# Optimization experiments

Hardware: AMD Instinct MI355X
Metric: run time of the kernel (lower is better)

The kernel has to match this reference:

```python
import jax, jax.numpy as jnp
import numpy as np

EPS = 1e-6

def masked_softmax(x, m, axis):
    # Faithful to KrantikariQA tensor_utils.masked_softmax:
    #   x = x*m; e = exp(x - max(x)) * m; e / (sum(e) + 1e-6)
    x = x * m
    ex = jnp.exp(x - jnp.max(x, axis=axis, keepdims=True)) * m
    return ex / (jnp.sum(ex, axis=axis, keepdims=True) + EPS)

def setup_inputs() -> dict:
    key = jax.random.key(0)
    k = jax.random.split(key, 7)
    Lq, Lp, B, D = 256, 256, 64, 1024
    q = jax.random.normal(k[0], (Lq, B, D), jnp.float32)
    p = jax.random.normal(k[1], (Lp, B, D), jnp.float32)
    qm = jax.random.randint(k[2], (B, Lq), 0, 2).astype(jnp.int32)
    pm = jax.random.randint(k[3], (B, Lp), 0, 2).astype(jnp.int32)
    # nn.Linear weights (out, in), no bias
    WF = jax.random.normal(k[4], (D, D), jnp.float32) * 0.02
    WG = jax.random.normal(k[5], (D, 2 * D), jnp.float32) * 0.02
    WH = jax.random.normal(k[6], (1, 2 * D), jnp.float32) * 0.02
    return {"q": q, "p": p, "qm": qm, "pm": pm, "WF": WF, "WG": WG, "WH": WH}

def reference(q, p, qm, pm, WF, WG, WH):
    # Attend: att = F(x), batch-first [B, L, D]
    att_q = jnp.einsum('lbd,ed->ble', q, WF)          # [B,Lq,D]
    att_p = jnp.einsum('lbd,ed->ble', p, WF)          # [B,Lp,D]
    e = jnp.einsum('bqe,bpe->bqp', att_q, att_p)      # [B,Lq,Lp]
    m = qm.astype(q.dtype)[:, :, None] * pm.astype(q.dtype)[:, None, :]  # [B,Lq,Lp]
    softmax_j = masked_softmax(e, m, axis=2)                              # over Lp
    softmax_i = masked_softmax(e.transpose(0, 2, 1), m.transpose(0, 2, 1), axis=2)  # [B,Lp,Lq]
    beta = jnp.einsum('bqp,pbd->bqd', softmax_j, p)   # [B,Lq,D]
    alpha = jnp.einsum('bpq,qbd->bpd', softmax_i, q)  # [B,Lp,D]
    # Compare
    v1 = jnp.concatenate([q.transpose(1, 0, 2), beta], axis=-1) @ WG.T   # [B,Lq,D]
    v2 = jnp.concatenate([p.transpose(1, 0, 2), alpha], axis=-1) @ WG.T  # [B,Lp,D]
    # Aggregate
    sum_v1 = jnp.sum(v1, axis=1)  # [B,D]
    sum_v2 = jnp.sum(v2, axis=1)  # [B,D]
    return jnp.concatenate([sum_v1, sum_v2], axis=-1) @ WH.T  # [B,1]
```

## Files before the change

kernel.cpp:

```cpp
#include <hip/hip_runtime.h>

typedef _Float16 f16x8 __attribute__((ext_vector_type(8)));
using f32x4 = __attribute__((ext_vector_type(4))) float;

constexpr int B = 64, L = 256, D = 1024;
constexpr int BD = B * D;
constexpr float EPS = 1e-6f;

__device__ __forceinline__ void gload_lds16(const void* g, void* l) {
    __builtin_amdgcn_global_load_lds((const __attribute__((address_space(1))) void*)g,
                                     (__attribute__((address_space(3))) void*)l,
                                     16, 0, 0);
}

__global__ __launch_bounds__(256) void k_wfgp(const float* __restrict__ WF,
                                              const float* __restrict__ WG,
                                              const float* __restrict__ WH,
                                              short* __restrict__ WFt16,
                                              float* __restrict__ gp1,
                                              float* __restrict__ gp2) {
    __shared__ float tile[32][33];
    const int bid = blockIdx.x;
    if (bid < 1024) {
        const int rt = bid >> 5, ct = bid & 31;
        const int t = threadIdx.x;
        const int r = t >> 3, c4 = (t & 7) * 4;
        float4 v = *(const float4*)(WF + (long)(rt * 32 + r) * D + ct * 32 + c4);
        tile[r][c4] = v.x; tile[r][c4 + 1] = v.y; tile[r][c4 + 2] = v.z; tile[r][c4 + 3] = v.w;
        __syncthreads();
        union { _Float16 h[4]; short4 s; } u;
        u.h[0] = (_Float16)tile[c4 + 0][r];
        u.h[1] = (_Float16)tile[c4 + 1][r];
        u.h[2] = (_Float16)tile[c4 + 2][r];
        u.h[3] = (_Float16)tile[c4 + 3][r];
        *(short4*)(WFt16 + (long)(ct * 32 + r) * D + rt * 32 + c4) = u.s;
    } else {
        const int lb = bid - 1024;
        const int kx = lb & 7, ec = lb >> 3;
        const int k = kx * 256 + threadIdx.x;
        const int e0 = ec * 128;
        float a = 0.f, c = 0.f;
        for (int e = 0; e < 128; ++e) {
            float w = WG[(long)(e0 + e) * (2 * D) + k];
            a += w * WH[e0 + e];
            c += w * WH[D + e0 + e];
        }
        gp1[ec * 2048 + k] = a; gp2[ec * 2048 + k] = c;
    }
}

template <int WM, int WN, int MR, int A32, int B32>
__global__ __launch_bounds__(WM * WN * 64) void k_gemm(
    const char* __restrict__ A, long sA, long bA,
    const char* __restrict__ Bm, long sB, long bB,
    int K, int bx, int per_batch, int f16_out,
    short* __restrict__ Ch, float* __restrict__ Cf, int ldC, long batchC)
{
    constexpr int BM = WM * MR * 16, BN = WN * 64;
    constexpr int T = WM * WN * 64;
    constexpr int TILEB = (BM + BN) * 64;
    constexpr int ROUNDS = TILEB / (T * 16);
    constexpr int ROUNDS_A = (BM * 4) / T;
    constexpr int R0 = A32 ? 0 : ROUNDS_A;
    constexpr int R1 = A32 ? ROUNDS_A : (B32 ? ROUNDS : ROUNDS_A);
    constexpr int NR = (R1 > R0) ? (R1 - R0) : 1;
    __shared__ __align__(16) char lds[2 * TILEB];

    const int t = threadIdx.x, lane = t & 63, w = t >> 6;
    const int wm = w / WN, wn = w % WN;

    const int lin = blockIdx.x;
    const int chunk = gridDim.x >> 3;
    const int swz = (lin & 7) * chunk + (lin >> 3);
    const int z = swz / per_batch;
    const int r0_ = swz % per_batch;
    const int mb = (r0_ / bx) * BM, nb = (r0_ % bx) * BN;

    const char* Ab = A + bA * z;
    const char* Bb = Bm + bB * z;

    const char* sp[ROUNDS];
    #pragma unroll
    for (int r = 0; r < ROUNDS; ++r) {
        int g = r * T + t;
        int row = g >> 2, sg = g & 3;
        int lg = sg ^ ((row >> 1) & 3);
        if (r < ROUNDS_A) sp[r] = Ab + (long)(mb + row) * sA + lg * (A32 ? 32 : 16);
        else              sp[r] = Bb + (long)(nb + row - BM) * sB + lg * (B32 ? 32 : 16);
    }

    int aoff[MR], boff[4];
    #pragma unroll
    for (int i = 0; i < MR; ++i) {
        int ra = wm * (MR * 16) + i * 16 + (lane & 15);
        aoff[i] = ra * 64 + (((lane >> 4) ^ ((ra >> 1) & 3))) * 16;
    }
    #pragma unroll
    for (int j = 0; j < 4; ++j) {
        int rb = wn * 64 + j * 16 + (lane & 15);
        boff[j] = BM * 64 + rb * 64 + (((lane >> 4) ^ ((rb >> 1) & 3))) * 16;
    }

    f32x4 acc[MR][4] = {};
    const int NT = K >> 5;
    int cur = 0;

#define CVT8(U, S0, S1)                                                     \
    U.h[0]=(_Float16)S0.x; U.h[1]=(_Float16)S0.y;                           \
    U.h[2]=(_Float16)S0.z; U.h[3]=(_Float16)S0.w;                           \
    U.h[4]=(_Float16)S1.x; U.h[5]=(_Float16)S1.y;                           \
    U.h[6]=(_Float16)S1.z; U.h[7]=(_Float16)S1.w;

#define GSTEP(WSRC, LDST, KT)                                               \
    {                                                                       \
        asm volatile("s_waitcnt vmcnt(0)" ::: "memory");                    \
        __builtin_amdgcn_sched_barrier(0);                                  \
        __builtin_amdgcn_s_barrier();                                       \
        __builtin_amdgcn_sched_barrier(0);                                  \
        char* dstb = lds + (cur ^ 1) * TILEB;                               \
        if ((KT) + 2 < NT) {                                                \
            long kb = (long)((KT) + 2) * 128;                               \
            _Pragma("unroll")                                               \
            for (int r = R0; r < R1; ++r) {                                 \
                LDST[r - R0][0] = *(const float4*)(sp[r] + kb);             \
                LDST[r - R0][1] = *(const float4*)(sp[r] + kb + 16);        \
            }                                                               \
        }                                                                   \
        if ((KT) + 1 < NT) {                                                \
            long kb16 = (long)((KT) + 1) * 64;                              \
            _Pragma("unroll")                                               \
            for (int r = 0; r < ROUNDS; ++r)                                \
                if (r < R0 || r >= R1)                                      \
                    gload_lds16(sp[r] + kb16, dstb + (r * T + t) * 16);     \
            _Pragma("unroll")                                               \
            for (int r = R0; r < R1; ++r) {                                 \
                union { _Float16 h[8]; int4 v; } u;                         \
                float4 s0 = WSRC[r - R0][0], s1 = WSRC[r - R0][1];          \
                CVT8(u, s0, s1)                                             \
                *((int4*)(dstb + (r * T + t) * 16)) = u.v;                  \
            }                                                               \
        }                                                                   \
        __builtin_amdgcn_sched_barrier(0);                                  \
        const char* lb = lds + cur * TILEB;                                 \
        f16x8 fb[4], fa[MR];                                                \
        _Pragma("unroll")                                                   \
        for (int j = 0; j < 4; ++j) fb[j] = *(const f16x8*)(lb + boff[j]);  \
        _Pragma("unroll")                                                   \
        for (int i = 0; i < MR; ++i) fa[i] = *(const f16x8*)(lb + aoff[i]); \
        _Pragma("unroll")                                                   \
        for (int i = 0; i < MR; ++i)                                        \
            _Pragma("unroll")                                               \
            for (int j = 0; j < 4; ++j)                                     \
                acc[i][j] = __builtin_amdgcn_mfma_f32_16x16x32_f16(         \
                    fb[j], fa[i], acc[i][j], 0, 0, 0);                      \
        asm volatile("s_waitcnt lgkmcnt(0)" ::: "memory");                  \
        __builtin_amdgcn_sched_barrier(0);                                  \
        cur ^= 1;                                                           \
    }

    if constexpr (A32 || B32) {
        float4 rsA[NR][2], rsB[NR][2];
        #pragma unroll
        for (int r = 0; r < ROUNDS; ++r) {
            if (r >= R0 && r < R1) {
                float4 s0 = *(const float4*)(sp[r]);
                float4 s1 = *(const float4*)(sp[r] + 16);
                union { _Float16 h[8]; int4 v; } u;
                CVT8(u, s0, s1)
                *((int4*)(lds + (r * T + t) * 16)) = u.v;
            } else {
                gload_lds16(sp[r], lds + (r * T + t) * 16);
            }
        }
        if (NT > 1) {
            #pragma unroll
            for (int r = R0; r < R1; ++r) {
                rsB[r - R0][0] = *(const float4*)(sp[r] + 128);
                rsB[r - R0][1] = *(const float4*)(sp[r] + 128 + 16);
            }
        }
        asm volatile("s_waitcnt lgkmcnt(0)" ::: "memory");
        for (int kt = 0; kt < NT; kt += 2) {
            GSTEP(rsB, rsA, kt)
            GSTEP(rsA, rsB, kt + 1)
        }
    } else {
        #pragma unroll
        for (int r = 0; r < ROUNDS; ++r)
            gload_lds16(sp[r], lds + (r * T + t) * 16);
        for (int kt = 0; kt < NT; ++kt) {
            asm volatile("s_waitcnt vmcnt(0)" ::: "memory");
            __builtin_amdgcn_sched_barrier(0);
            __builtin_amdgcn_s_barrier();
            __builtin_amdgcn_sched_barrier(0);
            if (kt + 1 < NT) {
                long kb = (long)(kt + 1) * 64;
                char* dstb = lds + (cur ^ 1) * TILEB;
                #pragma unroll
                for (int r = 0; r < ROUNDS; ++r)
                    gload_lds16(sp[r] + kb, dstb + (r * T + t) * 16);
            }
            __builtin_amdgcn_sched_barrier(0);
            const char* lb = lds + cur * TILEB;
            f16x8 fb[4], fa[MR];
            #pragma unroll
            for (int j = 0; j < 4; ++j) fb[j] = *(const f16x8*)(lb + boff[j]);
            #pragma unroll
            for (int i = 0; i < MR; ++i) fa[i] = *(const f16x8*)(lb + aoff[i]);
            #pragma unroll
            for (int i = 0; i < MR; ++i)
                #pragma unroll
                for (int j = 0; j < 4; ++j)
                    acc[i][j] = __builtin_amdgcn_mfma_f32_16x16x32_f16(fb[j], fa[i], acc[i][j], 0, 0, 0);
            cur ^= 1;
        }
    }
#undef GSTEP
#undef CVT8

    const long zC = batchC * z;
    #pragma unroll
    for (int i = 0; i < MR; ++i)
        #pragma unroll
        for (int j = 0; j < 4; ++j) {
            int row = mb + wm * (MR * 16) + i * 16 + (lane & 15);
            int col = nb + wn * 64 + j * 16 + (lane >> 4) * 4;
            long idx = zC + (long)row * ldC + col;
            if (f16_out) {
                union { _Float16 h[4]; short4 s; } u;
                #pragma unroll
                for (int rr = 0; rr < 4; ++rr) u.h[rr] = (_Float16)acc[i][j][rr];
                *(short4*)(Ch + idx) = u.s;
            } else {
                float4 v = make_float4(acc[i][j][0], acc[i][j][1], acc[i][j][2], acc[i][j][3]);
                *(float4*)(Cf + idx) = v;
            }
        }
}

__global__ __launch_bounds__(256) void k_fold_g(const float* __restrict__ Gp,
                                                short* __restrict__ G16) {
    const int i = blockIdx.x * 256 + threadIdx.x;
    constexpr int N4 = (1 << 20) / 4;
    const float4* g = (const float4*)Gp;
    float4 v0 = g[i], v1 = g[N4 + i], v2 = g[2 * N4 + i], v3 = g[3 * N4 + i];
    union { _Float16 h[4]; short4 s; } u;
    u.h[0] = (_Float16)(v0.x + v1.x + v2.x + v3.x);
    u.h[1] = (_Float16)(v0.y + v1.y + v2.y + v3.y);
    u.h[2] = (_Float16)(v0.z + v1.z + v2.z + v3.z);
    u.h[3] = (_Float16)(v0.w + v1.w + v2.w + v3.w);
    ((short4*)G16)[i] = u.s;
}

__global__ __launch_bounds__(256) void k_pass1(const float* __restrict__ E,
                                               const int* __restrict__ qm,
                                               const int* __restrict__ pm,
                                               float* __restrict__ impart,
                                               float* __restrict__ ispart,
                                               float* __restrict__ cjpart) {
    const int qc = blockIdx.x, b = blockIdx.y;
    const int p = threadIdx.x, lane = p & 63, w = p >> 6;
    const int q0 = qc * 32;
    __shared__ float wred[32][4];
    __shared__ float rowmx[32], rowsm[32], qmv_s[32];
    if (p < 32) qmv_s[p] = (float)qm[b * L + q0 + p];
    __syncthreads();
    const float pmv = (float)pm[b * L + p];
    const float* eb = E + b * (L * L) + q0 * L + p;

    float xv[32];
    float im = -1e30f;
    #pragma unroll
    for (int r = 0; r < 32; ++r) {
        float mm = pmv * qmv_s[r];
        float x = eb[r * L] * mm;
        xv[r] = x;
        im = fmaxf(im, x);
        float v = x;
        #pragma unroll
        for (int o = 32; o; o >>= 1) v = fmaxf(v, __shfl_xor(v, o));
        if (lane == 0) wred[r][w] = v;
    }
    __syncthreads();
    if (p < 32) rowmx[p] = fmaxf(fmaxf(wred[p][0], wred[p][1]), fmaxf(wred[p][2], wred[p][3]));
    __syncthreads();
    float is = 0.f;
    #pragma unroll
    for (int r = 0; r < 32; ++r) {
        float mm = pmv * qmv_s[r];
        is += mm * __expf(xv[r] - im);
        float v = mm * __expf(xv[r] - rowmx[r]);
        #pragma unroll
        for (int o = 32; o; o >>= 1) v += __shfl_xor(v, o);
        if (lane == 0) wred[r][w] = v;
    }
    __syncthreads();
    if (p < 32) rowsm[p] = wred[p][0] + wred[p][1] + wred[p][2] + wred[p][3];
    __syncthreads();
    float cj = 0.f;
    #pragma unroll
    for (int r = 0; r < 32; ++r) {
        float mm = pmv * qmv_s[r];
        cj += mm * __expf(xv[r] - rowmx[r]) / (rowsm[r] + EPS);
    }
    const int o = (b * 8 + qc) * 256 + p;
    impart[o] = im; ispart[o] = is; cjpart[o] = cj;
}

__global__ __launch_bounds__(256) void k_combine(const float* __restrict__ impart,
                                                 const float* __restrict__ ispart,
                                                 const float* __restrict__ cjpart,
                                                 float* __restrict__ rmi,
                                                 float* __restrict__ rsi,
                                                 float* __restrict__ colj) {
    const int b = blockIdx.x, p = threadIdx.x;
    const int base = b * 8 * 256 + p;
    float m = -1e30f, s = 0.f, c = 0.f;
    #pragma unroll
    for (int k = 0; k < 8; ++k) m = fmaxf(m, impart[base + k * 256]);
    #pragma unroll
    for (int k = 0; k < 8; ++k) {
        s += ispart[base + k * 256] * __expf(impart[base + k * 256] - m);
        c += cjpart[base + k * 256];
    }
    rmi[b * L + p] = m; rsi[b * L + p] = s; colj[b * L + p] = c;
}

__global__ __launch_bounds__(256) void k_colsum_i(const float* __restrict__ E,
                                                  const int* __restrict__ qm,
                                                  const int* __restrict__ pm,
                                                  const float* __restrict__ rmaxi,
                                                  const float* __restrict__ rsumi,
                                                  float* __restrict__ coli) {
    const int wid = threadIdx.x >> 6, lane = threadIdx.x & 63;
    const int row = blockIdx.x * 4 + wid;
    const int b = row >> 8;
    const float qmv = (float)qm[row];
    const float* er = E + row * L;
    float acc = 0.f;
    #pragma unroll
    for (int i = 0; i < 4; ++i) {
        int pp = lane + 64 * i;
        float mm = qmv * (float)pm[b * L + pp];
        float x = er[pp] * mm;
        acc += mm * __expf(x - rmaxi[b * L + pp]) / (rsumi[b * L + pp] + EPS);
    }
    #pragma unroll
    for (int o = 32; o; o >>= 1) acc += __shfl_xor(acc, o);
    if (lane == 0) coli[row] = acc;
}

__global__ __launch_bounds__(128) void k_sums2(const float* __restrict__ Q,
                                               const float* __restrict__ P,
                                               const float* __restrict__ colj,
                                               const float* __restrict__ coli,
                                               float* __restrict__ pq,
                                               float* __restrict__ pp,
                                               float* __restrict__ pb,
                                               float* __restrict__ pa) {
    const int c = blockIdx.x, b = blockIdx.y, t = threadIdx.x;
    const int d0 = t * 8;
    float aq[8] = {}, ap[8] = {}, ab[8] = {}, aa[8] = {};
    for (int l = c * 16; l < c * 16 + 16; ++l) {
        const float* qp = Q + (long)l * BD + b * D + d0;
        const float* pp_ = P + (long)l * BD + b * D + d0;
        float4 q0 = *(const float4*)qp, q1 = *(const float4*)(qp + 4);
        float4 p0 = *(const float4*)pp_, p1 = *(const float4*)(pp_ + 4);
        float cj = colj[b * L + l], ci = coli[b * L + l];
        float qv[8] = {q0.x, q0.y, q0.z, q0.w, q1.x, q1.y, q1.z, q1.w};
        float pv[8] = {p0.x, p0.y, p0.z, p0.w, p1.x, p1.y, p1.z, p1.w};
        #pragma unroll
        for (int k = 0; k < 8; ++k) {
            aq[k] += qv[k]; ap[k] += pv[k]; ab[k] += cj * pv[k]; aa[k] += ci * qv[k];
        }
    }
    const long o = ((long)c * B + b) * D + d0;
    *(float4*)(pq + o) = make_float4(aq[0], aq[1], aq[2], aq[3]);
    *(float4*)(pq + o + 4) = make_float4(aq[4], aq[5], aq[6], aq[7]);
    *(float4*)(pp + o) = make_float4(ap[0], ap[1], ap[2], ap[3]);
    *(float4*)(pp + o + 4) = make_float4(ap[4], ap[5], ap[6], ap[7]);
    *(float4*)(pb + o) = make_float4(ab[0], ab[1], ab[2], ab[3]);
    *(float4*)(pb + o + 4) = make_float4(ab[4], ab[5], ab[6], ab[7]);
    *(float4*)(pa + o) = make_float4(aa[0], aa[1], aa[2], aa[3]);
    *(float4*)(pa + o + 4) = make_float4(aa[4], aa[5], aa[6], aa[7]);
}

__global__ __launch_bounds__(256) void k_final2(const float* __restrict__ pq,
                                                const float* __restrict__ pp,
                                                const float* __restrict__ pb,
                                                const float* __restrict__ pa,
                                                const float* __restrict__ gp1,
                                                const float* __restrict__ gp2,
                                                float* __restrict__ out) {
    const int b = blockIdx.x, t = threadIdx.x;
    float acc = 0.f;
    for (int d = t; d < D; d += 256) {
        float sq = 0.f, sp_ = 0.f, sb = 0.f, sa = 0.f;
        #pragma unroll
        for (int c2 = 0; c2 < 16; ++c2) {
            long o = ((long)c2 * B + b) * D + d;
            sq += pq[o]; sp_ += pp[o]; sb += pb[o]; sa += pa[o];
        }
        float g1d = 0.f, g1D = 0.f, g2d = 0.f, g2D = 0.f;
        #pragma unroll
        for (int ec = 0; ec < 8; ++ec) {
            g1d += gp1[ec * 2048 + d];     g1D += gp1[ec * 2048 + D + d];
            g2d += gp2[ec * 2048 + d];     g2D += gp2[ec * 2048 + D + d];
        }
        acc += sq * g1d + sb * g1D + sp_ * g2d + sa * g2D;
    }
    #pragma unroll
    for (int o = 32; o; o >>= 1) acc += __shfl_xor(acc, o);
    __shared__ float red[4];
    const int wid = t >> 6, lane = t & 63;
    if (lane == 0) red[wid] = acc;
    __syncthreads();
    if (t == 0) out[b] = red[0] + red[1] + red[2] + red[3];
}

extern "C" void kernel_launch(void* const* d_in, const int* in_sizes, int n_in,
                              void* d_out, int out_size, void* d_ws, size_t ws_size,
                              hipStream_t stream) {
    const float* q  = (const float*)d_in[0];
    const float* p  = (const float*)d_in[1];
    const int*   qm = (const int*)d_in[2];
    const int*   pm = (const int*)d_in[3];
    const float* WF = (const float*)d_in[4];
    const float* WG = (const float*)d_in[5];
    const float* WH = (const float*)d_in[6];
    float* out = (float*)d_out;

    char* wsb = (char*)d_ws;
    short* T16   = (short*)(wsb);
    short* WFt16 = (short*)(wsb + (32l << 20));
    short* G16   = (short*)(wsb + (34l << 20));
    float* Gp    = (float*)(wsb + (36l << 20));
    float* E     = (float*)(wsb + (36l << 20));
    float* st    = (float*)(wsb + (52l << 20));
    const int BL = B * L;
    float* impart = st;                  float* ispart = impart + B * 8 * 256;
    float* cjpart = ispart + B * 8 * 256;
    float* rmi  = cjpart + B * 8 * 256;  float* rsi  = rmi + BL;
    float* colj = rsi + BL;              float* coli = colj + BL;
    float* pq   = coli + BL;             float* pp   = pq + 16 * BD;
    float* pb   = pp + 16 * BD;          float* pa   = pb + 16 * BD;
    float* gp1  = pa + 16 * BD;          float* gp2  = gp1 + 8 * 2048;

    k_wfgp<<<1088, 256, 0, stream>>>(WF, WG, WH, WFt16, gp1, gp2);
    k_gemm<2, 2, 4, 0, 0><<<256, 256, 0, stream>>>(
        (const char*)WFt16, 2048, 512, (const char*)WFt16, 2048, 512,
        256, 8, 64, 0, nullptr, Gp, 1024, 1l << 20);
    k_fold_g<<<1024, 256, 0, stream>>>(Gp, G16);
    k_gemm<2, 4, 8, 1, 0><<<256, 512, 0, stream>>>(
        (const char*)q, 4096, 0, (const char*)G16, 2048, 0,
        1024, 4, 256, 1, T16, nullptr, 1024, 0);
    k_gemm<2, 2, 4, 0, 1><<<256, 256, 0, stream>>>(
        (const char*)T16, 64l * 2048, 2048, (const char*)p, 64l * 4096, 4096,
        1024, 2, 4, 0, nullptr, E, 256, 65536);
    k_pass1<<<dim3(8, B), 256, 0, stream>>>(E, qm, pm, impart, ispart, cjpart);
    k_combine<<<B, 256, 0, stream>>>(impart, ispart, cjpart, rmi, rsi, colj);
    k_colsum_i<<<BL / 4, 256, 0, stream>>>(E, qm, pm, rmi, rsi, coli);
    k_sums2<<<dim3(16, B), 128, 0, stream>>>(q, p, colj, coli, pq, pp, pb, pa);
    k_final2<<<B, 256, 0, stream>>>(pq, pp, pb, pa, gp1, gp2, out);
}
```

Baseline: 190.2 us.

## Triple-buffer GEMM LDS pipeline with two-tile lookahead and partial vmcnt waits

Replaces the double-buffered GEMM main loop with a three-stage LDS ring. Loads are issued two k-tiles ahead, and the loop waits with a partial vmcnt so the next tile's loads stay in flight during compute. The fp32 register-staged convert path and the direct global-to-LDS path now share one loop. In exchange it uses 50% more LDS per block, which may reduce occupancy, and it relies on hard-coded vmcnt counts matching the number of issued loads.

```diff
diff --git a/kernel.cpp b/kernel.cpp
--- a/kernel.cpp
+++ b/kernel.cpp
@@ -63,8 +63,11 @@
     constexpr int ROUNDS_A = (BM * 4) / T;
     constexpr int R0 = A32 ? 0 : ROUNDS_A;
     constexpr int R1 = A32 ? ROUNDS_A : (B32 ? ROUNDS : ROUNDS_A);
-    constexpr int NR = (R1 > R0) ? (R1 - R0) : 1;
-    __shared__ __align__(16) char lds[2 * TILEB];
+    constexpr int NF32 = (R1 > R0) ? (R1 - R0) : 0;
+    constexpr int NRS = NF32 ? NF32 : 1;
+    constexpr int VSET = (ROUNDS - NF32) + 2 * NF32;
+    static_assert(VSET == 4 || VSET == 6, "vmcnt literal dispatch");
+    __shared__ __align__(16) char lds[3 * TILEB];
 
     const int t = threadIdx.x, lane = t & 63, w = t >> 6;
     const int wm = w / WN, wn = w % WN;
@@ -103,45 +106,43 @@
 
     f32x4 acc[MR][4] = {};
     const int NT = K >> 5;
-    int cur = 0;
-
-#define CVT8(U, S0, S1)                                                     \
-    U.h[0]=(_Float16)S0.x; U.h[1]=(_Float16)S0.y;                           \
-    U.h[2]=(_Float16)S0.z; U.h[3]=(_Float16)S0.w;                           \
-    U.h[4]=(_Float16)S1.x; U.h[5]=(_Float16)S1.y;                           \
-    U.h[6]=(_Float16)S1.z; U.h[7]=(_Float16)S1.w;
-
-#define GSTEP(WSRC, LDST, KT)                                               \
+    float4 rsE[NRS][2], rsO[NRS][2];
+
+#define ISSUE(KT, RS)                                                       \
     {                                                                       \
-        asm volatile("s_waitcnt vmcnt(0)" ::: "memory");                    \
+        char* dstb = lds + ((KT) % 3) * TILEB;                              \
+        long kb16 = (long)(KT) * 64, kb32 = (long)(KT) * 128;               \
+        _Pragma("unroll")                                                   \
+        for (int r = 0; r < ROUNDS; ++r)                                    \
+            if (r < R0 || r >= R1)                                          \
+                gload_lds16(sp[r] + kb16, dstb + (r * T + t) * 16);         \
+        _Pragma("unroll")                                                   \
+        for (int r = R0; r < R1; ++r) {                                     \
+            RS[r - R0][0] = *(const float4*)(sp[r] + kb32);                 \
+            RS[r - R0][1] = *(const float4*)(sp[r] + kb32 + 16);            \
+        }                                                                   \
+    }
+
+#define CVTW(KT, RS)                                                        \
+    if (NF32) {                                                             \
+        char* dstb = lds + ((KT) % 3) * TILEB;                              \
+        _Pragma("unroll")                                                   \
+        for (int r = R0; r < R1; ++r) {                                     \
+            union { _Float16 h[8]; int4 v; } u;                             \
+            float4 s0 = RS[r - R0][0], s1 = RS[r - R0][1];                  \
+            u.h[0]=(_Float16)s0.x; u.h[1]=(_Float16)s0.y;                   \
+            u.h[2]=(_Float16)s0.z; u.h[3]=(_Float16)s0.w;                   \
+            u.h[4]=(_Float16)s1.x; u.h[5]=(_Float16)s1.y;                   \
+            u.h[6]=(_Float16)s1.z; u.h[7]=(_Float16)s1.w;                   \
+            *((int4*)(dstb + (r * T + t) * 16)) = u.v;                      \
+        }                                                                   \
+        asm volatile("s_waitcnt lgkmcnt(0)" ::: "memory");                  \
         __builtin_amdgcn_sched_barrier(0);                                  \
-        __builtin_amdgcn_s_barrier();                                       \
-        __builtin_amdgcn_sched_barrier(0);                                  \
-        char* dstb = lds + (cur ^ 1) * TILEB;                               \
-        if ((KT) + 2 < NT) {                                                \
-            long kb = (long)((KT) + 2) * 128;                               \
-            _Pragma("unroll")                                               \
-            for (int r = R0; r < R1; ++r) {                                 \
-                LDST[r - R0][0] = *(const float4*)(sp[r] + kb);             \
-                LDST[r - R0][1] = *(const float4*)(sp[r] + kb + 16);        \
-            }                                                               \
-        }                                                                   \
-        if ((KT) + 1 < NT) {                                                \
-            long kb16 = (long)((KT) + 1) * 64;                              \
-            _Pragma("unroll")                                               \
-            for (int r = 0; r < ROUNDS; ++r)                                \
-                if (r < R0 || r >= R1)                                      \
-                    gload_lds16(sp[r] + kb16, dstb + (r * T + t) * 16);     \
-            _Pragma("unroll")                                               \
-            for (int r = R0; r < R1; ++r) {                                 \
-                union { _Float16 h[8]; int4 v; } u;                         \
-                float4 s0 = WSRC[r - R0][0], s1 = WSRC[r - R0][1];          \
-                CVT8(u, s0, s1)                                             \
-                *((int4*)(dstb + (r * T + t) * 16)) = u.v;                  \
-            }                                                               \
-        }                                                                   \
-        __builtin_amdgcn_sched_barrier(0);                                  \
-        const char* lb = lds + cur * TILEB;                                 \
+    }
+
+#define COMPUTE(KT)                                                         \
+    {                                                                       \
+        const char* lb = lds + ((KT) % 3) * TILEB;                          \
         f16x8 fb[4], fa[MR];                                                \
         _Pragma("unroll")                                                   \
         for (int j = 0; j < 4; ++j) fb[j] = *(const f16x8*)(lb + boff[j]);  \
@@ -153,70 +154,37 @@
             for (int j = 0; j < 4; ++j)                                     \
                 acc[i][j] = __builtin_amdgcn_mfma_f32_16x16x32_f16(         \
                     fb[j], fa[i], acc[i][j], 0, 0, 0);                      \
-        asm volatile("s_waitcnt lgkmcnt(0)" ::: "memory");                  \
+    }
+
+#define STEP(KT, RS)                                                        \
+    {                                                                       \
+        if ((KT) + 1 < NT) {                                                \
+            if constexpr (VSET == 4)                                        \
+                asm volatile("s_waitcnt vmcnt(4)" ::: "memory");            \
+            else                                                            \
+                asm volatile("s_waitcnt vmcnt(6)" ::: "memory");            \
+        } else {                                                            \
+            asm volatile("s_waitcnt vmcnt(0)" ::: "memory");                \
+        }                                                                   \
         __builtin_amdgcn_sched_barrier(0);                                  \
-        cur ^= 1;                                                           \
-    }
-
-    if constexpr (A32 || B32) {
-        float4 rsA[NR][2], rsB[NR][2];
-        #pragma unroll
-        for (int r = 0; r < ROUNDS; ++r) {
-            if (r >= R0 && r < R1) {
-                float4 s0 = *(const float4*)(sp[r]);
-                float4 s1 = *(const float4*)(sp[r] + 16);
-                union { _Float16 h[8]; int4 v; } u;
-                CVT8(u, s0, s1)
-                *((int4*)(lds + (r * T + t) * 16)) = u.v;
-            } else {
-                gload_lds16(sp[r], lds + (r * T + t) * 16);
-            }
-        }
-        if (NT > 1) {
-            #pragma unroll
-            for (int r = R0; r < R1; ++r) {
-                rsB[r - R0][0] = *(const float4*)(sp[r] + 128);
-                rsB[r - R0][1] = *(const float4*)(sp[r] + 128 + 16);
-            }
-        }
-        asm volatile("s_waitcnt lgkmcnt(0)" ::: "memory");
-        for (int kt = 0; kt < NT; kt += 2) {
-            GSTEP(rsB, rsA, kt)
-            GSTEP(rsA, rsB, kt + 1)
-        }
-    } else {
-        #pragma unroll
-        for (int r = 0; r < ROUNDS; ++r)
-            gload_lds16(sp[r], lds + (r * T + t) * 16);
-        for (int kt = 0; kt < NT; ++kt) {
-            asm volatile("s_waitcnt vmcnt(0)" ::: "memory");
-            __builtin_amdgcn_sched_barrier(0);
-            __builtin_amdgcn_s_barrier();
-            __builtin_amdgcn_sched_barrier(0);
-            if (kt + 1 < NT) {
-                long kb = (long)(kt + 1) * 64;
-                char* dstb = lds + (cur ^ 1) * TILEB;
-                #pragma unroll
-                for (int r = 0; r < ROUNDS; ++r)
-                    gload_lds16(sp[r] + kb, dstb + (r * T + t) * 16);
-            }
-            __builtin_amdgcn_sched_barrier(0);
-            const char* lb = lds + cur * TILEB;
-            f16x8 fb[4], fa[MR];
-            #pragma unroll
-            for (int j = 0; j < 4; ++j) fb[j] = *(const f16x8*)(lb + boff[j]);
-            #pragma unroll
-            for (int i = 0; i < MR; ++i) fa[i] = *(const f16x8*)(lb + aoff[i]);
-            #pragma unroll
-            for (int i = 0; i < MR; ++i)
-                #pragma unroll
-                for (int j = 0; j < 4; ++j)
-                    acc[i][j] = __builtin_amdgcn_mfma_f32_16x16x32_f16(fb[j], fa[i], acc[i][j], 0, 0, 0);
-            cur ^= 1;
-        }
-    }
-#undef GSTEP
-#undef CVT8
+        CVTW(KT, RS)                                                        \
+        __builtin_amdgcn_s_barrier();                                       \
+        __builtin_amdgcn_sched_barrier(0);                                  \
+        if ((KT) + 2 < NT) ISSUE((KT) + 2, RS)                              \
+        __builtin_amdgcn_sched_barrier(0);                                  \
+        COMPUTE(KT)                                                         \
+    }
+
+    ISSUE(0, rsE)
+    ISSUE(1, rsO)
+    for (int kt = 0; kt < NT; kt += 2) {
+        STEP(kt, rsE)
+        STEP(kt + 1, rsO)
+    }
+#undef STEP
+#undef COMPUTE
+#undef CVTW
+#undef ISSUE
 
     const long zC = batchC * z;
     #pragma unroll
```

Measured after the change: 163.9 us. 1.16x faster.
